# Kernel optimization log

Hardware: AMD Instinct MI355X
Metric: run time of the kernel (lower is better)

The kernel has to match this reference:

```python
import jax, jax.numpy as jnp
import numpy as np

B, L, D = 4, 4096, 128
BLOCK, SPARSITY = 64, 0.9
NEG = -1e9


def _make_block_mask(key):
    nb = L // BLOCK
    bm = jax.random.uniform(key, (nb, nb)) > SPARSITY
    bm = bm | jnp.eye(nb, dtype=bool)  # keep diagonal blocks so no row is fully masked
    bm = jnp.tril(bm)
    return jnp.repeat(jnp.repeat(bm, BLOCK, axis=0), BLOCK, axis=1)  # [L, L]


def _xavier(key, shape):
    limit = float(np.sqrt(6.0 / (shape[0] + shape[1])))
    return jax.random.uniform(key, shape, jnp.float32, -limit, limit)


def setup_inputs() -> dict:
    key = jax.random.key(0)
    ks = jax.random.split(key, 10)
    t = lambda k: jax.random.normal(k, (B, L, D), jnp.float32)
    return {
        'q_real': t(ks[0]), 'q_imag': t(ks[1]),
        'k_real': t(ks[2]), 'k_imag': t(ks[3]),
        'v_real': t(ks[4]), 'v_imag': t(ks[5]),
        'W_qkv': _xavier(ks[6], (6 * D, 6 * D)),
        'b_qkv': jnp.zeros((6 * D,), jnp.float32),
        'W_out': _xavier(ks[7], (2 * D, 2 * D)),
        'b_out': jnp.zeros((2 * D,), jnp.float32),
        'block_mask': _make_block_mask(ks[8]),
    }


def reference(q_real, q_imag, k_real, k_imag, v_real, v_imag,
              W_qkv, b_qkv, W_out, b_out, block_mask):
    d = q_real.shape[-1]
    scale = d ** -0.5
    # fused qkv projection over the 6 concatenated channels
    x = jnp.concatenate([q_real, q_imag, k_real, k_imag, v_real, v_imag], axis=-1)  # [B,L,6D]
    qkv = (x @ W_qkv.T + b_qkv).reshape(x.shape[0], x.shape[1], 6, d)
    q_r, q_i, k_r, k_i, v_r, v_i = (qkv[:, :, j] for j in range(6))

    def attn(q, k, v):
        s = jnp.einsum('bqd,bkd->bqk', q, k) * scale          # [B,L,L]
        s = jnp.where(block_mask[None], s, NEG)               # block-sparse mask
        a = jax.nn.softmax(s, axis=-1)                        # dropout = identity (eval)
        return jnp.einsum('bqk,bkd->bqd', a, v)

    out = jnp.concatenate([attn(q_r, k_r, v_r), attn(q_i, k_i, v_i)], axis=-1)  # [B,L,2D]
    out = out @ W_out.T + b_out
    return out[..., :d], out[..., d:]
```

## Files before the change

### kernel.cpp

```cpp
#include <hip/hip_runtime.h>
#include <hip/hip_bf16.h>

typedef unsigned short u16;
typedef __attribute__((ext_vector_type(8))) short bf16x8;
typedef __attribute__((ext_vector_type(4))) float f32x4;

#define SEQ_L 4096
#define M_TOT 16384

__device__ __forceinline__ float bf2f(u16 x) {
    unsigned u = ((unsigned)x) << 16;
    return __builtin_bit_cast(float, u);
}
__device__ __forceinline__ u16 f2bf(float f) {
    unsigned u = __builtin_bit_cast(unsigned, f);
    u += 0x7FFFu + ((u >> 16) & 1u);
    return (u16)(u >> 16);
}
__device__ __forceinline__ void gload16(const u16* g, u16* l) {
    __builtin_amdgcn_global_load_lds(
        (const __attribute__((address_space(1))) unsigned int*)g,
        (__attribute__((address_space(3))) unsigned int*)l, 16, 0, 0);
}

__global__ __launch_bounds__(256) void prep_all(
    const float* __restrict__ in0, const float* __restrict__ in1, const float* __restrict__ in2,
    const float* __restrict__ in3, const float* __restrict__ in4, const float* __restrict__ in5,
    const float* __restrict__ Wqkv, const float* __restrict__ Wout, const void* __restrict__ mask,
    u16* __restrict__ x, u16* __restrict__ Wqkv_bf, u16* __restrict__ Wout_bf,
    unsigned long long* __restrict__ bmap) {
    int id = blockIdx.x * 256 + threadIdx.x;
    if (id < 1572864) {
        const float* ins[6] = {in0, in1, in2, in3, in4, in5};
        int which = id >> 18, j = id & 262143;
        int m = j >> 4, c8 = j & 15;
        const float* sp = ins[which] + (size_t)m * 128 + c8 * 8;
        float4 a = *(const float4*)sp;
        float4 b = *(const float4*)(sp + 4);
        u16 t[8] = {f2bf(a.x), f2bf(a.y), f2bf(a.z), f2bf(a.w),
                    f2bf(b.x), f2bf(b.y), f2bf(b.z), f2bf(b.w)};
        *(uint4*)(x + (size_t)m * 768 + which * 128 + c8 * 8) = *(uint4*)t;
    } else if (id < 1572864 + 73728 + 8192) {
        int i = id - 1572864;
        const float* src = (i < 73728) ? Wqkv : Wout;
        u16* dst = (i < 73728) ? Wqkv_bf : Wout_bf;
        if (i >= 73728) i -= 73728;
        const float* sp = src + (size_t)i * 8;
        float4 a = *(const float4*)sp;
        float4 b = *(const float4*)(sp + 4);
        u16 t[8] = {f2bf(a.x), f2bf(a.y), f2bf(a.z), f2bf(a.w),
                    f2bf(b.x), f2bf(b.y), f2bf(b.z), f2bf(b.w)};
        *(uint4*)(dst + (size_t)i * 8) = *(uint4*)t;
    } else if (id < 1572864 + 73728 + 8192 + 4096) {
        int i = id - 1572864 - 73728 - 8192;
        int bi = i >> 6, bj = i & 63;
        size_t e = (size_t)(bi * 64) * SEQ_L + (size_t)bj * 64;
        const unsigned char* p8 = (const unsigned char*)mask;
        unsigned w0 = *(const unsigned*)mask;
        bool v;
        if (w0 == 0x01010101u || w0 == 0xFFFFFFFFu)      v = p8[e] != 0;
        else if (w0 == 0x3F803F80u || w0 == 0x3C003C00u) v = ((const u16*)mask)[e] != 0;
        else                                             v = ((const unsigned*)mask)[e] != 0;
        unsigned long long bits = __ballot(v);
        if ((i & 63) == 0) bmap[bi] = bits;
    }
}

__global__ __launch_bounds__(256, 4) void qkv_gemm(
    const u16* __restrict__ X, const u16* __restrict__ W, const float* __restrict__ bias,
    u16* __restrict__ qk, u16* __restrict__ vt) {
    __shared__ __align__(16) u16 As[128 * 64];
    __shared__ __align__(16) u16 Bs[64 * 64];
    int m0 = blockIdx.x * 128, n0 = blockIdx.y * 64;
    int tid = threadIdx.x, lane = tid & 63, w = tid >> 6;
    int ln = lane & 15, quad = lane >> 4;
    int rw = (w >> 1) * 64, cw = (w & 1) * 32;
    int lr8 = lane >> 3, lc = lane & 7;
    f32x4 acc[4][2] = {};
    for (int kk = 0; kk < 768; kk += 64) {
        __syncthreads();
        #pragma unroll
        for (int j = 0; j < 4; j++) {
            int r0 = w * 32 + j * 8, r = r0 + lr8;
            gload16(X + (size_t)(m0 + r) * 768 + kk + ((lc ^ (r & 7)) * 8), As + r0 * 64 + lane * 8);
        }
        #pragma unroll
        for (int j = 0; j < 2; j++) {
            int r0 = w * 16 + j * 8, r = r0 + lr8;
            gload16(W + (size_t)(n0 + r) * 768 + kk + ((lc ^ (r & 7)) * 8), Bs + r0 * 64 + lane * 8);
        }
        __syncthreads();
        #pragma unroll
        for (int s = 0; s < 2; s++) {
            bf16x8 af[4], bfr[2];
            #pragma unroll
            for (int i = 0; i < 4; i++) {
                int R = rw + i * 16 + ln;
                af[i] = *(const bf16x8*)(As + R * 64 + ((4 * s + quad) ^ (ln & 7)) * 8);
            }
            #pragma unroll
            for (int t = 0; t < 2; t++) {
                int R = cw + t * 16 + ln;
                bfr[t] = *(const bf16x8*)(Bs + R * 64 + ((4 * s + quad) ^ (ln & 7)) * 8);
            }
            #pragma unroll
            for (int i = 0; i < 4; i++)
                #pragma unroll
                for (int t = 0; t < 2; t++)
                    acc[i][t] = __builtin_amdgcn_mfma_f32_16x16x32_bf16(af[i], bfr[t], acc[i][t], 0, 0, 0);
        }
    }
    #pragma unroll
    for (int i = 0; i < 4; i++) {
        int row0 = m0 + rw + i * 16 + 4 * quad;
        #pragma unroll
        for (int t = 0; t < 2; t++) {
            int col = n0 + cw + t * 16 + ln;
            float bv = bias[col];
            if (col < 512) {
                #pragma unroll
                for (int r = 0; r < 4; r++)
                    qk[(size_t)(row0 + r) * 512 + col] = f2bf(acc[i][t][r] + bv);
            } else {
                int d = col - 512;
                int b = row0 >> 12, seq = row0 & 4095;
                u16 pk[4] = {f2bf(acc[i][t][0] + bv), f2bf(acc[i][t][1] + bv),
                             f2bf(acc[i][t][2] + bv), f2bf(acc[i][t][3] + bv)};
                *(ushort4*)(vt + ((size_t)(b * 2 + (d >> 7)) * 128 + (d & 127)) * SEQ_L + seq)
                    = *(ushort4*)pk;
            }
        }
    }
}

__global__ __launch_bounds__(256, 2) void attn_sparse(
    const u16* __restrict__ qk, const u16* __restrict__ vt,
    const unsigned long long* __restrict__ bmap, u16* __restrict__ attn_bf) {
    __shared__ __align__(16) u16 Ksm[4][32 * 128];
    __shared__ __align__(16) u16 Vsm[4][128 * 32];
    __shared__ __align__(16) u16 Psm[4][16 * 40];

    int lane = threadIdx.x & 63, w = threadIdx.x >> 6;
    int ln = lane & 15, quad = lane >> 4;
    int g = blockIdx.x * 4 + w;
    int u = g >> 5, v = g & 31;
    int qi = (u < 32) ? (63 - u) : (u - 32);
    int b = v >> 3, ch = (v >> 2) & 1, quarter = v & 3;
    int rowbase = b * SEQ_L + qi * 64 + quarter * 16;
    const float scale = 0.08838834764831845f;

    u16* K = Ksm[w];
    u16* V = Vsm[w];
    u16* Ps = Psm[w];

    bf16x8 qf[4];
    {
        const u16* qp = qk + (size_t)(rowbase + ln) * 512 + ch * 128;
        #pragma unroll
        for (int s = 0; s < 4; s++) qf[s] = *(const bf16x8*)(qp + 32 * s + 8 * quad);
    }
    float m_st[4], l_st[4];
    #pragma unroll
    for (int r = 0; r < 4; r++) { m_st[r] = -1e30f; l_st[r] = 0.f; }
    f32x4 accO[8] = {};

    const u16* kbase0 = qk + (size_t)b * SEQ_L * 512 + 256 + ch * 128;
    const u16* vbase0 = vt + (size_t)(b * 2 + ch) * 128 * SEQ_L;
    unsigned long long bm = bmap[qi];

    while (bm) {
        int kb = __ffsll(bm) - 1; bm &= bm - 1;
        #pragma unroll
        for (int sub = 0; sub < 2; sub++) {
            const u16* kp = kbase0 + (size_t)(kb * 64 + sub * 32) * 512;
            const u16* vp = vbase0 + kb * 64 + sub * 32;
            #pragma unroll
            for (int j = 0; j < 8; j++) {
                int kr = j * 4 + (lane >> 4);
                gload16(kp + (size_t)kr * 512 + (((lane & 15) ^ (kr & 7)) * 8),
                        K + j * 4 * 128 + lane * 8);
            }
            #pragma unroll
            for (int j = 0; j < 8; j++) {
                int d = j * 16 + (lane >> 2);
                gload16(vp + (size_t)d * SEQ_L + (((lane & 3) ^ (d & 3)) * 8),
                        V + j * 16 * 32 + lane * 8);
            }
            __builtin_amdgcn_s_waitcnt(0x0F78);

            f32x4 accS[2] = {};
            #pragma unroll
            for (int s = 0; s < 4; s++)
                #pragma unroll
                for (int t = 0; t < 2; t++) {
                    bf16x8 kf = *(const bf16x8*)(K + (t * 16 + ln) * 128 +
                                                 (((4 * s + quad) ^ (ln & 7)) * 8));
                    accS[t] = __builtin_amdgcn_mfma_f32_16x16x32_bf16(qf[s], kf, accS[t], 0, 0, 0);
                }

            #pragma unroll
            for (int r = 0; r < 4; r++) {
                float s0 = accS[0][r] * scale, s1 = accS[1][r] * scale;
                float mx = fmaxf(s0, s1);
                #pragma unroll
                for (int off = 1; off < 16; off <<= 1) mx = fmaxf(mx, __shfl_xor(mx, off, 64));
                float nm = fmaxf(m_st[r], mx);
                float alpha = __expf(m_st[r] - nm);
                m_st[r] = nm;
                float p0 = __expf(s0 - nm), p1 = __expf(s1 - nm);
                Ps[(4 * quad + r) * 40 + ln] = f2bf(p0);
                Ps[(4 * quad + r) * 40 + ln + 16] = f2bf(p1);
                float rs = p0 + p1;
                #pragma unroll
                for (int off = 1; off < 16; off <<= 1) rs += __shfl_xor(rs, off, 64);
                l_st[r] = l_st[r] * alpha + rs;
                #pragma unroll
                for (int nt = 0; nt < 8; nt++) accO[nt][r] *= alpha;
            }

            __builtin_amdgcn_s_waitcnt(0x0F70);
            bf16x8 pf = *(const bf16x8*)(Ps + ln * 40 + 8 * quad);
            #pragma unroll
            for (int nt = 0; nt < 8; nt++) {
                bf16x8 vf = *(const bf16x8*)(V + (nt * 16 + ln) * 32 +
                                             ((quad ^ (ln & 3)) * 8));
                accO[nt] = __builtin_amdgcn_mfma_f32_16x16x32_bf16(pf, vf, accO[nt], 0, 0, 0);
            }
        }
    }

    float inv[4];
    #pragma unroll
    for (int r = 0; r < 4; r++) inv[r] = 1.0f / fmaxf(l_st[r], 1e-20f);
    #pragma unroll
    for (int nt = 0; nt < 8; nt++)
        #pragma unroll
        for (int r = 0; r < 4; r++)
            attn_bf[(size_t)(rowbase + 4 * quad + r) * 256 + ch * 128 + nt * 16 + ln]
                = f2bf(accO[nt][r] * inv[r]);
}

__global__ __launch_bounds__(256) void out_gemm(
    const u16* __restrict__ A, const u16* __restrict__ W, const float* __restrict__ bias,
    float* __restrict__ out) {
    __shared__ __align__(16) u16 As[64 * 64];
    __shared__ __align__(16) u16 Bs[64 * 64];
    int m0 = blockIdx.x * 64, n0 = blockIdx.y * 64;
    int tid = threadIdx.x, lane = tid & 63, w = tid >> 6;
    int ln = lane & 15, quad = lane >> 4;
    int lr8 = lane >> 3, lc = lane & 7;
    int swz_st = lc ^ (lr8 & 7);
    f32x4 acc[4] = {};
    for (int kk = 0; kk < 256; kk += 64) {
        __syncthreads();
        #pragma unroll
        for (int j = 0; j < 2; j++) {
            int r0 = w * 16 + j * 8;
            int r = r0 + lr8;
            gload16(A + (size_t)(m0 + r) * 256 + kk + swz_st * 8, As + r0 * 64 + lane * 8);
            gload16(W + (size_t)(n0 + r) * 256 + kk + swz_st * 8, Bs + r0 * 64 + lane * 8);
        }
        __syncthreads();
        #pragma unroll
        for (int s = 0; s < 2; s++) {
            int R = w * 16 + ln;
            bf16x8 af = *(const bf16x8*)(As + R * 64 + ((4 * s + quad) ^ (ln & 7)) * 8);
            #pragma unroll
            for (int t = 0; t < 4; t++) {
                int Rb = t * 16 + ln;
                bf16x8 bfr = *(const bf16x8*)(Bs + Rb * 64 + ((4 * s + quad) ^ (ln & 7)) * 8);
                acc[t] = __builtin_amdgcn_mfma_f32_16x16x32_bf16(af, bfr, acc[t], 0, 0, 0);
            }
        }
    }
    const size_t half = (size_t)M_TOT * 128;
    #pragma unroll
    for (int t = 0; t < 4; t++) {
        int col = n0 + t * 16 + ln;
        float bv = bias[col];
        float* base = (col < 128) ? (out + col) : (out + half + (col - 128));
        #pragma unroll
        for (int r = 0; r < 4; r++) {
            int row = m0 + w * 16 + 4 * quad + r;
            base[(size_t)row * 128] = acc[t][r] + bv;
        }
    }
}

extern "C" void kernel_launch(void* const* d_in, const int* in_sizes, int n_in,
                              void* d_out, int out_size, void* d_ws, size_t ws_size,
                              hipStream_t stream) {
    char* ws = (char*)d_ws;
    u16* x_bf    = (u16*)ws;
    u16* qk_buf  = x_bf + (size_t)M_TOT * 768;
    u16* vt_buf  = qk_buf + (size_t)M_TOT * 512;
    u16* attn_bf = vt_buf + (size_t)1024 * SEQ_L;
    u16* Wqkv_bf = attn_bf + (size_t)M_TOT * 256;
    u16* Wout_bf = Wqkv_bf + 589824;
    unsigned long long* bmap = (unsigned long long*)(Wout_bf + 65536);

    hipLaunchKernelGGL(prep_all, dim3(6480), dim3(256), 0, stream,
                       (const float*)d_in[0], (const float*)d_in[1], (const float*)d_in[2],
                       (const float*)d_in[3], (const float*)d_in[4], (const float*)d_in[5],
                       (const float*)d_in[6], (const float*)d_in[8], d_in[10],
                       x_bf, Wqkv_bf, Wout_bf, bmap);
    hipLaunchKernelGGL(qkv_gemm, dim3(128, 12), dim3(256), 0, stream,
                       x_bf, Wqkv_bf, (const float*)d_in[7], qk_buf, vt_buf);
    hipLaunchKernelGGL(attn_sparse, dim3(512), dim3(256), 0, stream,
                       qk_buf, vt_buf, bmap, attn_bf);
    hipLaunchKernelGGL(out_gemm, dim3(256, 4), dim3(256), 0, stream,
                       attn_bf, Wout_bf, (const float*)d_in[9], (float*)d_out);
}
```

Measured before the change: 217.0 us.

## Share K/V tiles across waves with double-buffered prefetch in sparse attention

The four waves of a block now work on the same (batch, channel, query block) and split its 64 query rows, so K/V tiles are loaded once cooperatively into shared LDS instead of once per wave. The next key block is prefetched into a second buffer while the current one is computed, and the loop now handles full 64-key blocks. The row sum is accumulated with an MFMA against a ones vector instead of shuffle reductions, and the max reductions are batched. This adds block-wide barriers and a different grid mapping, which could cause waves to stall on each other.

```diff
diff --git a/kernel.cpp b/kernel.cpp
--- a/kernel.cpp
+++ b/kernel.cpp
@@ -136,21 +136,17 @@
 __global__ __launch_bounds__(256, 2) void attn_sparse(
     const u16* __restrict__ qk, const u16* __restrict__ vt,
     const unsigned long long* __restrict__ bmap, u16* __restrict__ attn_bf) {
-    __shared__ __align__(16) u16 Ksm[4][32 * 128];
-    __shared__ __align__(16) u16 Vsm[4][128 * 32];
-    __shared__ __align__(16) u16 Psm[4][16 * 40];
+    __shared__ __align__(16) u16 Ks[2][64 * 128];
+    __shared__ __align__(16) u16 Vs[2][128 * 64];
+    __shared__ __align__(16) u16 Psm[4][16 * 72];
 
     int lane = threadIdx.x & 63, w = threadIdx.x >> 6;
     int ln = lane & 15, quad = lane >> 4;
-    int g = blockIdx.x * 4 + w;
-    int u = g >> 5, v = g & 31;
+    int u = blockIdx.x >> 3, v = blockIdx.x & 7;
     int qi = (u < 32) ? (63 - u) : (u - 32);
-    int b = v >> 3, ch = (v >> 2) & 1, quarter = v & 3;
-    int rowbase = b * SEQ_L + qi * 64 + quarter * 16;
+    int b = v >> 1, ch = v & 1;
+    int rowbase = b * SEQ_L + qi * 64 + w * 16;
     const float scale = 0.08838834764831845f;
-
-    u16* K = Ksm[w];
-    u16* V = Vsm[w];
     u16* Ps = Psm[w];
 
     bf16x8 qf[4];
@@ -159,79 +155,131 @@
         #pragma unroll
         for (int s = 0; s < 4; s++) qf[s] = *(const bf16x8*)(qp + 32 * s + 8 * quad);
     }
-    float m_st[4], l_st[4];
-    #pragma unroll
-    for (int r = 0; r < 4; r++) { m_st[r] = -1e30f; l_st[r] = 0.f; }
+    bf16x8 onesb;
+    #pragma unroll
+    for (int j = 0; j < 8; j++) onesb[j] = (short)0x3F80;
+
+    float m_st[4];
+    #pragma unroll
+    for (int r = 0; r < 4; r++) m_st[r] = -1e30f;
     f32x4 accO[8] = {};
+    f32x4 accL = {};
 
     const u16* kbase0 = qk + (size_t)b * SEQ_L * 512 + 256 + ch * 128;
     const u16* vbase0 = vt + (size_t)(b * 2 + ch) * 128 * SEQ_L;
     unsigned long long bm = bmap[qi];
 
-    while (bm) {
-        int kb = __ffsll(bm) - 1; bm &= bm - 1;
-        #pragma unroll
-        for (int sub = 0; sub < 2; sub++) {
-            const u16* kp = kbase0 + (size_t)(kb * 64 + sub * 32) * 512;
-            const u16* vp = vbase0 + kb * 64 + sub * 32;
-            #pragma unroll
-            for (int j = 0; j < 8; j++) {
-                int kr = j * 4 + (lane >> 4);
+    int kb = __ffsll(bm) - 1; bm &= bm - 1;
+    {
+        const u16* kp = kbase0 + (size_t)(kb * 64) * 512;
+        const u16* vp = vbase0 + kb * 64;
+        #pragma unroll
+        for (int j = 0; j < 4; j++) {
+            int kr = w * 16 + j * 4 + (lane >> 4);
+            gload16(kp + (size_t)kr * 512 + (((lane & 15) ^ (kr & 7)) * 8),
+                    Ks[0] + (w * 16 + j * 4) * 128 + lane * 8);
+        }
+        #pragma unroll
+        for (int j = 0; j < 4; j++) {
+            int d = w * 32 + j * 8 + (lane >> 3);
+            gload16(vp + (size_t)d * SEQ_L + (((lane & 7) ^ (d & 7)) * 8),
+                    Vs[0] + (w * 32 + j * 8) * 64 + lane * 8);
+        }
+    }
+
+    int bufc = 0;
+    while (true) {
+        int nkb = -1;
+        if (bm) {
+            nkb = __ffsll(bm) - 1; bm &= bm - 1;
+            const u16* kp = kbase0 + (size_t)(nkb * 64) * 512;
+            const u16* vp = vbase0 + nkb * 64;
+            u16* Kd = Ks[bufc ^ 1];
+            u16* Vd = Vs[bufc ^ 1];
+            #pragma unroll
+            for (int j = 0; j < 4; j++) {
+                int kr = w * 16 + j * 4 + (lane >> 4);
                 gload16(kp + (size_t)kr * 512 + (((lane & 15) ^ (kr & 7)) * 8),
-                        K + j * 4 * 128 + lane * 8);
-            }
-            #pragma unroll
-            for (int j = 0; j < 8; j++) {
-                int d = j * 16 + (lane >> 2);
-                gload16(vp + (size_t)d * SEQ_L + (((lane & 3) ^ (d & 3)) * 8),
-                        V + j * 16 * 32 + lane * 8);
-            }
-            __builtin_amdgcn_s_waitcnt(0x0F78);
-
-            f32x4 accS[2] = {};
-            #pragma unroll
-            for (int s = 0; s < 4; s++)
-                #pragma unroll
-                for (int t = 0; t < 2; t++) {
-                    bf16x8 kf = *(const bf16x8*)(K + (t * 16 + ln) * 128 +
-                                                 (((4 * s + quad) ^ (ln & 7)) * 8));
-                    accS[t] = __builtin_amdgcn_mfma_f32_16x16x32_bf16(qf[s], kf, accS[t], 0, 0, 0);
-                }
-
-            #pragma unroll
-            for (int r = 0; r < 4; r++) {
-                float s0 = accS[0][r] * scale, s1 = accS[1][r] * scale;
-                float mx = fmaxf(s0, s1);
-                #pragma unroll
-                for (int off = 1; off < 16; off <<= 1) mx = fmaxf(mx, __shfl_xor(mx, off, 64));
-                float nm = fmaxf(m_st[r], mx);
-                float alpha = __expf(m_st[r] - nm);
-                m_st[r] = nm;
-                float p0 = __expf(s0 - nm), p1 = __expf(s1 - nm);
-                Ps[(4 * quad + r) * 40 + ln] = f2bf(p0);
-                Ps[(4 * quad + r) * 40 + ln + 16] = f2bf(p1);
-                float rs = p0 + p1;
-                #pragma unroll
-                for (int off = 1; off < 16; off <<= 1) rs += __shfl_xor(rs, off, 64);
-                l_st[r] = l_st[r] * alpha + rs;
-                #pragma unroll
-                for (int nt = 0; nt < 8; nt++) accO[nt][r] *= alpha;
-            }
-
-            __builtin_amdgcn_s_waitcnt(0x0F70);
-            bf16x8 pf = *(const bf16x8*)(Ps + ln * 40 + 8 * quad);
+                        Kd + (w * 16 + j * 4) * 128 + lane * 8);
+            }
+            #pragma unroll
+            for (int j = 0; j < 4; j++) {
+                int d = w * 32 + j * 8 + (lane >> 3);
+                gload16(vp + (size_t)d * SEQ_L + (((lane & 7) ^ (d & 7)) * 8),
+                        Vd + (w * 32 + j * 8) * 64 + lane * 8);
+            }
+        }
+        if (nkb >= 0) __builtin_amdgcn_s_waitcnt(0x0F78);
+        else          __builtin_amdgcn_s_waitcnt(0x0F70);
+        __builtin_amdgcn_s_barrier();
+
+        const u16* K = Ks[bufc];
+        const u16* V = Vs[bufc];
+
+        f32x4 accS[4] = {};
+        #pragma unroll
+        for (int s = 0; s < 4; s++)
+            #pragma unroll
+            for (int t = 0; t < 4; t++) {
+                bf16x8 kf = *(const bf16x8*)(K + (t * 16 + ln) * 128 +
+                                             (((4 * s + quad) ^ (ln & 7)) * 8));
+                accS[t] = __builtin_amdgcn_mfma_f32_16x16x32_bf16(qf[s], kf, accS[t], 0, 0, 0);
+            }
+
+        float mx[4];
+        #pragma unroll
+        for (int r = 0; r < 4; r++)
+            mx[r] = fmaxf(fmaxf(accS[0][r], accS[1][r]),
+                          fmaxf(accS[2][r], accS[3][r])) * scale;
+        #pragma unroll
+        for (int off = 1; off < 16; off <<= 1) {
+            float t0 = __shfl_xor(mx[0], off, 64);
+            float t1 = __shfl_xor(mx[1], off, 64);
+            float t2 = __shfl_xor(mx[2], off, 64);
+            float t3 = __shfl_xor(mx[3], off, 64);
+            mx[0] = fmaxf(mx[0], t0); mx[1] = fmaxf(mx[1], t1);
+            mx[2] = fmaxf(mx[2], t2); mx[3] = fmaxf(mx[3], t3);
+        }
+        float alpha[4];
+        #pragma unroll
+        for (int r = 0; r < 4; r++) {
+            float nm = fmaxf(m_st[r], mx[r]);
+            alpha[r] = __expf(m_st[r] - nm);
+            m_st[r] = nm;
+        }
+        #pragma unroll
+        for (int r = 0; r < 4; r++)
+            #pragma unroll
+            for (int t = 0; t < 4; t++)
+                Ps[(4 * quad + r) * 72 + t * 16 + ln] =
+                    f2bf(__expf(accS[t][r] * scale - m_st[r]));
+        #pragma unroll
+        for (int nt = 0; nt < 8; nt++)
+            #pragma unroll
+            for (int r = 0; r < 4; r++) accO[nt][r] *= alpha[r];
+        #pragma unroll
+        for (int r = 0; r < 4; r++) accL[r] *= alpha[r];
+
+        #pragma unroll
+        for (int h = 0; h < 2; h++) {
+            bf16x8 pf = *(const bf16x8*)(Ps + ln * 72 + h * 32 + 8 * quad);
+            accL = __builtin_amdgcn_mfma_f32_16x16x32_bf16(pf, onesb, accL, 0, 0, 0);
             #pragma unroll
             for (int nt = 0; nt < 8; nt++) {
-                bf16x8 vf = *(const bf16x8*)(V + (nt * 16 + ln) * 32 +
-                                             ((quad ^ (ln & 3)) * 8));
+                bf16x8 vf = *(const bf16x8*)(V + (nt * 16 + ln) * 64 +
+                                             (((4 * h + quad) ^ (ln & 7)) * 8));
                 accO[nt] = __builtin_amdgcn_mfma_f32_16x16x32_bf16(pf, vf, accO[nt], 0, 0, 0);
             }
         }
+
+        if (nkb < 0) break;
+        __builtin_amdgcn_s_barrier();
+        bufc ^= 1;
     }
 
     float inv[4];
     #pragma unroll
-    for (int r = 0; r < 4; r++) inv[r] = 1.0f / fmaxf(l_st[r], 1e-20f);
+    for (int r = 0; r < 4; r++) inv[r] = 1.0f / fmaxf(accL[r], 1e-20f);
     #pragma unroll
     for (int nt = 0; nt < 8; nt++)
         #pragma unroll
```

Result: faster. 202.8 us (-6.6%).
